# Optimization experiments

Hardware: AMD Instinct MI355X
Metric: run time of the kernel (lower is better)

The kernel has to match this reference:

```python
import jax, jax.numpy as jnp
import numpy as np

TOP_K = 2

def setup_inputs() -> dict:
    key = jax.random.key(0)
    ks = jax.random.split(key, 5)
    B, T, C, E, H = 4, 2048, 1024, 16, 4096
    x = jax.random.normal(ks[0], (B, T, C), dtype=jnp.float32)
    w_router = jax.random.normal(ks[1], (C, E), dtype=jnp.float32) / np.sqrt(C)
    w1 = jax.random.normal(ks[2], (E, C, H), dtype=jnp.float32) / np.sqrt(C)
    b1 = jnp.zeros((E, H), dtype=jnp.float32)
    w2 = jax.random.normal(ks[3], (E, H, C), dtype=jnp.float32) / np.sqrt(H)
    b2 = jnp.zeros((E, C), dtype=jnp.float32)
    return {"x": x, "w_router": w_router, "w1": w1, "b1": b1, "w2": w2, "b2": b2}


def reference(x, w_router, w1, b1, w2, b2):
    B, T, C = x.shape
    E = w1.shape[0]
    xf = x.reshape(-1, C)                       # [N, C]
    N = xf.shape[0]

    logits = xf @ w_router                      # [N, E]
    rw, sel = jax.lax.top_k(logits, TOP_K)      # [N, K]
    rw = jax.nn.softmax(rw.astype(jnp.float32), axis=-1).astype(x.dtype)

    # combine weight per (token, expert): sum of routing weights over the
    # k-slots that selected that expert (equivalent to the per-k masked loop)
    comb = jnp.zeros((N, E), dtype=x.dtype)
    comb = comb.at[jnp.arange(N)[:, None], sel].add(rw)  # [N, E]

    # loop over experts via scan: out += comb[:, e:e+1] * FFN_e(xf)
    def step(acc, params):
        w1e, b1e, w2e, b2e, ce = params         # ce: [N]
        h = jax.nn.relu(xf @ w1e + b1e)         # [N, 4C]
        y = h @ w2e + b2e                       # [N, C]
        return acc + ce[:, None] * y, None

    out0 = jnp.zeros_like(xf)
    out, _ = jax.lax.scan(step, out0, (w1, b1, w2, b2, comb.T))
    return out.reshape(B, T, C)
```

## Files before the change

### kernel.cpp

```cpp
#include <hip/hip_runtime.h>
#include <hip/hip_bf16.h>


typedef __attribute__((ext_vector_type(4))) float f32x4;
typedef __attribute__((ext_vector_type(8))) __bf16 bf16x8;
typedef __attribute__((ext_vector_type(8))) unsigned short u16x8;

#define NEXP 16
#define CAP  2048
#define CDIM 1024
#define HDIM 4096
#define KS2 2
#define BMG 256
#define BNG 256
#define SLOT 8192

__device__ __forceinline__ unsigned short f2bf(float f) {
  return __builtin_bit_cast(unsigned short, (__bf16)f);
}

typedef __attribute__((address_space(3))) void  lds_void;
typedef __attribute__((address_space(1))) const void gbl_void;
__device__ __forceinline__ void gload16(const void* g, void* l) {
  __builtin_amdgcn_global_load_lds((gbl_void*)g, (lds_void*)l, 16, 0, 0);
}

__device__ __forceinline__ void xcd_remap(int& bx, int& by, int& bz) {
  const int gx = gridDim.x, gy = gridDim.y;
  const int nwg = gx * gy * gridDim.z;
  int flat = blockIdx.x + gx * (blockIdx.y + gy * blockIdx.z);
  flat = (flat & 7) * (nwg >> 3) + (flat >> 3);
  bx = flat % gx;
  const int t = flat / gx;
  by = t % gy;
  bz = t / gy;
}

__global__ __launch_bounds__(64) void router_kernel(
    const float* __restrict__ x, const float* __restrict__ wr,
    float* __restrict__ pair_w, int* __restrict__ counts,
    int* __restrict__ lists)
{
  const int n = blockIdx.x;
  const int l = threadIdx.x;
  const float* xrow = x + (size_t)n * CDIM;
  double acc[NEXP];
#pragma unroll
  for (int e = 0; e < NEXP; e++) acc[e] = 0.0;
  for (int it = 0; it < CDIM / 64; it++) {
    const int c = l + it * 64;
    const double xv = (double)xrow[c];
    const float* w = wr + c * NEXP;
#pragma unroll
    for (int e = 0; e < NEXP; e++) acc[e] += xv * (double)w[e];
  }
#pragma unroll
  for (int e = 0; e < NEXP; e++) {
    double v = acc[e];
    for (int off = 32; off > 0; off >>= 1) v += __shfl_xor(v, off, 64);
    acc[e] = v;
  }
  if (l == 0) {
    int e0 = 0; double b0 = acc[0];
    for (int e = 1; e < NEXP; e++) if (acc[e] > b0) { b0 = acc[e]; e0 = e; }
    int e1 = -1; double b1v = -1e300;
    for (int e = 0; e < NEXP; e++) {
      if (e == e0) continue;
      if (acc[e] > b1v) { b1v = acc[e]; e1 = e; }
    }
    const double d = exp(b1v - b0);
    pair_w[2 * n]     = (float)(1.0 / (1.0 + d));
    pair_w[2 * n + 1] = (float)(d / (1.0 + d));
    int p0 = atomicAdd(&counts[e0], 1);
    if (p0 < CAP) lists[e0 * CAP + p0] = 2 * n;
    int p1 = atomicAdd(&counts[e1], 1);
    if (p1 < CAP) lists[e1 * CAP + p1] = 2 * n + 1;
  }
}

__global__ __launch_bounds__(256) void cvt_x_kernel(
    const float* __restrict__ x, unsigned short* __restrict__ xb, int n8)
{
  const int i = blockIdx.x * 256 + threadIdx.x;
  if (i >= n8) return;
  float4 a = ((const float4*)x)[2 * i];
  float4 b = ((const float4*)x)[2 * i + 1];
  u16x8 v;
  v[0] = f2bf(a.x); v[1] = f2bf(a.y); v[2] = f2bf(a.z); v[3] = f2bf(a.w);
  v[4] = f2bf(b.x); v[5] = f2bf(b.y); v[6] = f2bf(b.z); v[7] = f2bf(b.w);
  ((u16x8*)xb)[i] = v;
}

__global__ __launch_bounds__(256) void transpose_cvt_kernel(
    const float* __restrict__ src, unsigned short* __restrict__ dst,
    int K, int Nn)
{
  __shared__ __align__(16) unsigned short tile[64][72];
  const size_t eoff = (size_t)blockIdx.z * K * Nn;
  const float* S = src + eoff;
  unsigned short* D = dst + eoff;
  const int n0 = blockIdx.x * 64, k0 = blockIdx.y * 64;
  const int t = threadIdx.x;
  {
    const int nl = (t & 15) * 4, kr = t >> 4;
#pragma unroll
    for (int p = 0; p < 4; p++) {
      const int k = kr + p * 16;
      float4 v = *(const float4*)(S + (size_t)(k0 + k) * Nn + n0 + nl);
      tile[nl + 0][k] = f2bf(v.x);
      tile[nl + 1][k] = f2bf(v.y);
      tile[nl + 2][k] = f2bf(v.z);
      tile[nl + 3][k] = f2bf(v.w);
    }
  }
  __syncthreads();
  {
    const int kq = (t & 7) * 8, nr = t >> 3;
#pragma unroll
    for (int p = 0; p < 2; p++) {
      const int n = nr + p * 32;
      u16x8 v = *(const u16x8*)&tile[n][kq];
      *(u16x8*)(D + (size_t)(n0 + n) * K + k0 + kq) = v;
    }
  }
}


#define STAGE(parx, hx, koffb)                                                 \
  do {                                                                         \
    unsigned short* Ad = &lds[((parx) * 2 + (hx)) * SLOT + w * 512];           \
    unsigned short* Bd = &lds[4 * SLOT + ((parx) * 2 + (hx)) * SLOT + w * 512];\
    gload16(agA0 + (koffb), Ad);                                               \
    gload16(agA1 + (koffb), Ad + 4096);                                        \
    gload16(bgB0 + (koffb), Bd);                                               \
    gload16(bgB1 + (koffb), Bd + 4096);                                        \
  } while (0)

#define COMPUTE(parx, hx)                                                      \
  do {                                                                         \
    const unsigned short* As_ = &lds[((parx) * 2 + (hx)) * SLOT];              \
    const unsigned short* Bs_ = &lds[4 * SLOT + ((parx) * 2 + (hx)) * SLOT];   \
    bf16x8 af[8], bfv[4];                                                      \
    _Pragma("unroll")                                                          \
    for (int mf = 0; mf < 8; mf++)                                             \
      af[mf] = *(const bf16x8*)(As_ + (wr * 128 + mf * 16 + lrow) * 32 + qsw); \
    _Pragma("unroll")                                                          \
    for (int nf = 0; nf < 4; nf++)                                             \
      bfv[nf] = *(const bf16x8*)(Bs_ + (wc * 64 + nf * 16 + lrow) * 32 + qsw); \
    __builtin_amdgcn_s_setprio(1);                                             \
    _Pragma("unroll")                                                          \
    for (int mf = 0; mf < 8; mf++)                                             \
      _Pragma("unroll")                                                        \
      for (int nf = 0; nf < 4; nf++)                                           \
        acc[mf][nf] = __builtin_amdgcn_mfma_f32_16x16x32_bf16(                 \
            af[mf], bfv[nf], acc[mf][nf], 0, 0, 0);                            \
    __builtin_amdgcn_s_setprio(0);                                             \
  } while (0)

#define VMCNT4 asm volatile("s_waitcnt vmcnt(4)" ::: "memory")
#define VMCNT0 asm volatile("s_waitcnt vmcnt(0)" ::: "memory")
#define SBAR   asm volatile("s_barrier" ::: "memory")

__global__ __launch_bounds__(512, 2) void gemm1_8p_kernel(
    const unsigned short* __restrict__ xb, const unsigned short* __restrict__ wb,
    const float* __restrict__ b1, const int* __restrict__ counts,
    const int* __restrict__ lists, unsigned short* __restrict__ Hb)
{
  int bx, by, bz;
  xcd_remap(bx, by, bz);
  const int e = bz;
  int cnt = counts[e]; if (cnt > CAP) cnt = CAP;
  const int m0 = by * BMG;
  if (m0 >= cnt) return;
  const int n0 = bx * BNG;
  const int* list = lists + e * CAP;
  const unsigned short* W = wb + (size_t)e * CDIM * HDIM;

  __shared__ __align__(16) unsigned short lds[8 * SLOT];

  const int t = threadIdx.x, w = t >> 6, lane = t & 63;
  const int wr = w >> 2, wc = w & 3;
  const int lrow = lane & 15, lgrp = lane >> 4;
  const int qsw = (lgrp ^ ((lrow >> 1) & 3)) * 8;

  const int sr0 = w * 16 + (lane >> 2), sr1 = 128 + w * 16 + (lane >> 2);
  const int sq = ((lane & 3) ^ ((lane >> 3) & 3)) * 16;
  int ai0 = m0 + sr0; if (ai0 > cnt - 1) ai0 = cnt - 1;
  int ai1 = m0 + sr1; if (ai1 > cnt - 1) ai1 = cnt - 1;
  const char* agA0 = (const char*)(xb + (size_t)(list[ai0] >> 1) * CDIM) + sq;
  const char* agA1 = (const char*)(xb + (size_t)(list[ai1] >> 1) * CDIM) + sq;
  const char* bgB0 = (const char*)(W + (size_t)(n0 + sr0) * CDIM) + sq;
  const char* bgB1 = (const char*)(W + (size_t)(n0 + sr1) * CDIM) + sq;

  f32x4 acc[8][4] = {};

  const int NT = CDIM / 64;
  STAGE(0, 0, 0);
  STAGE(0, 1, 64);
  for (int tt = 0; tt < NT - 1; ++tt) {
    const int par = tt & 1;
    const int kofn = (tt + 1) * 128;
#pragma unroll
    for (int h = 0; h < 2; ++h) {
      VMCNT4; SBAR;
      STAGE(par ^ 1, h, kofn + h * 64);
      COMPUTE(par, h);
    }
  }
  {
    const int par = (NT - 1) & 1;
    VMCNT4; SBAR; COMPUTE(par, 0);
    VMCNT0; SBAR; COMPUTE(par, 1);
  }

  int hrow[8][4]; bool valid[8][4];
#pragma unroll
  for (int mf = 0; mf < 8; mf++)
#pragma unroll
    for (int rr = 0; rr < 4; rr++) {
      const int mi = m0 + wr * 128 + mf * 16 + lgrp * 4 + rr;
      valid[mf][rr] = (mi < cnt);
      hrow[mf][rr] = list[valid[mf][rr] ? mi : (cnt - 1)];
    }
#pragma unroll
  for (int nf = 0; nf < 4; nf++) {
    const int col = n0 + wc * 64 + nf * 16 + lrow;
    const float bias = b1[e * HDIM + col];
#pragma unroll
    for (int mf = 0; mf < 8; mf++)
#pragma unroll
      for (int rr = 0; rr < 4; rr++)
        if (valid[mf][rr]) {
          float h = acc[mf][nf][rr] + bias;
          h = h > 0.f ? h : 0.f;
          Hb[(size_t)hrow[mf][rr] * HDIM + col] = f2bf(h);
        }
  }
}

__global__ __launch_bounds__(512, 2) void gemm2_8p_kernel(
    const unsigned short* __restrict__ Hb, const unsigned short* __restrict__ wb,
    const float* __restrict__ b2, const float* __restrict__ pair_w,
    const int* __restrict__ counts, const int* __restrict__ lists,
    float* __restrict__ out)
{
  int bx, by, bz;
  xcd_remap(bx, by, bz);
  const int e = bz / KS2, ks = bz % KS2;
  int cnt = counts[e]; if (cnt > CAP) cnt = CAP;
  const int m0 = by * BMG;
  if (m0 >= cnt) return;
  const int n0 = bx * BNG;
  const int* list = lists + e * CAP;
  const unsigned short* W = wb + (size_t)e * HDIM * CDIM;
  const int kbegb = ks * (HDIM / KS2) * 2;

  __shared__ __align__(16) unsigned short lds[8 * SLOT];

  const int t = threadIdx.x, w = t >> 6, lane = t & 63;
  const int wr = w >> 2, wc = w & 3;
  const int lrow = lane & 15, lgrp = lane >> 4;
  const int qsw = (lgrp ^ ((lrow >> 1) & 3)) * 8;

  const int sr0 = w * 16 + (lane >> 2), sr1 = 128 + w * 16 + (lane >> 2);
  const int sq = ((lane & 3) ^ ((lane >> 3) & 3)) * 16;
  int ai0 = m0 + sr0; if (ai0 > cnt - 1) ai0 = cnt - 1;
  int ai1 = m0 + sr1; if (ai1 > cnt - 1) ai1 = cnt - 1;
  const char* agA0 = (const char*)(Hb + (size_t)list[ai0] * HDIM) + kbegb + sq;
  const char* agA1 = (const char*)(Hb + (size_t)list[ai1] * HDIM) + kbegb + sq;
  const char* bgB0 = (const char*)(W + (size_t)(n0 + sr0) * HDIM) + kbegb + sq;
  const char* bgB1 = (const char*)(W + (size_t)(n0 + sr1) * HDIM) + kbegb + sq;

  f32x4 acc[8][4] = {};

  const int NT = (HDIM / KS2) / 64;
  STAGE(0, 0, 0);
  STAGE(0, 1, 64);
  for (int tt = 0; tt < NT - 1; ++tt) {
    const int par = tt & 1;
    const int kofn = (tt + 1) * 128;
#pragma unroll
    for (int h = 0; h < 2; ++h) {
      VMCNT4; SBAR;
      STAGE(par ^ 1, h, kofn + h * 64);
      COMPUTE(par, h);
    }
  }
  {
    const int par = (NT - 1) & 1;
    VMCNT4; SBAR; COMPUTE(par, 0);
    VMCNT0; SBAR; COMPUTE(par, 1);
  }

  float wgt[8][4]; int tok[8][4]; bool valid[8][4];
#pragma unroll
  for (int mf = 0; mf < 8; mf++)
#pragma unroll
    for (int rr = 0; rr < 4; rr++) {
      const int mi = m0 + wr * 128 + mf * 16 + lgrp * 4 + rr;
      valid[mf][rr] = (mi < cnt);
      const int p = list[valid[mf][rr] ? mi : (cnt - 1)];
      wgt[mf][rr] = pair_w[p];
      tok[mf][rr] = p >> 1;
    }
#pragma unroll
  for (int nf = 0; nf < 4; nf++) {
    const int col = n0 + wc * 64 + nf * 16 + lrow;
    const float bias = (ks == 0) ? b2[e * CDIM + col] : 0.f;
#pragma unroll
    for (int mf = 0; mf < 8; mf++)
#pragma unroll
      for (int rr = 0; rr < 4; rr++)
        if (valid[mf][rr])
          atomicAdd(out + (size_t)tok[mf][rr] * CDIM + col,
                    wgt[mf][rr] * (acc[mf][nf][rr] + bias));
  }
}

__device__ __forceinline__ int swz(int row, int b) {
  return row * 128 + (b ^ (((row >> 1) & 7) << 4));
}

#define MFMA_COMPUTE_F(Abase, Bbase)                                           \
  _Pragma("unroll")                                                            \
  for (int kk = 0; kk < 2; kk++) {                                             \
    bf16x8 af[4], bfr[4];                                                      \
    const int kb = (kk * 32 + lgrp * 8) * 2;                                   \
    _Pragma("unroll")                                                          \
    for (int i = 0; i < 4; i++)                                                \
      af[i] = *(const bf16x8*)((Abase) + swz(wm + i * 16 + lrow, kb));         \
    _Pragma("unroll")                                                          \
    for (int j = 0; j < 4; j++)                                                \
      bfr[j] = *(const bf16x8*)((Bbase) + swz(wn + j * 16 + lrow, kb));        \
    _Pragma("unroll")                                                          \
    for (int i = 0; i < 4; i++)                                                \
      _Pragma("unroll")                                                        \
      for (int j = 0; j < 4; j++)                                              \
        acc[i][j] = __builtin_amdgcn_mfma_f32_16x16x32_bf16(                   \
            af[i], bfr[j], acc[i][j], 0, 0, 0);                                \
  }

__global__ __launch_bounds__(256) void gemm1_f32_kernel(
    const float* __restrict__ x, const float* __restrict__ w1,
    const float* __restrict__ b1, const int* __restrict__ counts,
    const int* __restrict__ lists, unsigned short* __restrict__ Hb,
    int e_base, int h_by_pair)
{
  const int e = e_base + blockIdx.z;
  int cnt = counts[e]; if (cnt > CAP) cnt = CAP;
  const int m0 = blockIdx.y * 128;
  if (m0 >= cnt) return;
  const int n0 = blockIdx.x * 128;
  const int* list = lists + e * CAP;
  const float* W = w1 + (size_t)e * CDIM * HDIM;
  __shared__ __align__(16) unsigned short As[128 * 64];
  __shared__ __align__(16) unsigned short Bs[128 * 64];
  const int t = threadIdx.x;
  const int a_row = t >> 1, a_half = t & 1;
  int a_idx = m0 + a_row; if (a_idx > cnt - 1) a_idx = cnt - 1;
  const float* a_src = x + (size_t)(list[a_idx] >> 1) * CDIM + a_half * 32;
  const int b_np = t & 63, b_kg = t >> 6;
  const int wid = t >> 6, lane = t & 63;
  const int wm = (wid >> 1) * 64, wn = (wid & 1) * 64;
  const int lrow = lane & 15, lgrp = lane >> 4;
  f32x4 acc[4][4] = {};
  for (int kt = 0; kt < CDIM; kt += 64) {
    {
      const float* s = a_src + kt;
      u16x8 cv[4];
#pragma unroll
      for (int q = 0; q < 4; q++) {
        float4 v0 = *(const float4*)(s + q * 8);
        float4 v1 = *(const float4*)(s + q * 8 + 4);
        cv[q][0] = f2bf(v0.x); cv[q][1] = f2bf(v0.y);
        cv[q][2] = f2bf(v0.z); cv[q][3] = f2bf(v0.w);
        cv[q][4] = f2bf(v1.x); cv[q][5] = f2bf(v1.y);
        cv[q][6] = f2bf(v1.z); cv[q][7] = f2bf(v1.w);
      }
#pragma unroll
      for (int q = 0; q < 4; q++)
        *(u16x8*)((char*)As + swz(a_row, (a_half * 32 + q * 8) * 2)) = cv[q];
    }
    {
#pragma unroll
      for (int it = 0; it < 2; it++) {
        const int k0 = (b_kg + 4 * it) * 8;
        u16x8 c0, c1;
#pragma unroll
        for (int j = 0; j < 8; j++) {
          float2 v = *(const float2*)(W + (size_t)(kt + k0 + j) * HDIM + n0 + 2 * b_np);
          c0[j] = f2bf(v.x); c1[j] = f2bf(v.y);
        }
        *(u16x8*)((char*)Bs + swz(2 * b_np,     k0 * 2)) = c0;
        *(u16x8*)((char*)Bs + swz(2 * b_np + 1, k0 * 2)) = c1;
      }
    }
    __syncthreads();
    MFMA_COMPUTE_F((const char*)As, (const char*)Bs)
    __syncthreads();
  }
  int hrow[4][4]; bool valid[4][4];
#pragma unroll
  for (int i = 0; i < 4; i++)
#pragma unroll
    for (int r = 0; r < 4; r++) {
      const int mi = m0 + wm + i * 16 + lgrp * 4 + r;
      valid[i][r] = (mi < cnt);
      const int idx = valid[i][r] ? mi : (cnt - 1);
      hrow[i][r] = h_by_pair ? list[idx] : idx;
    }
#pragma unroll
  for (int j = 0; j < 4; j++) {
    const int col = n0 + wn + j * 16 + lrow;
    const float bias = b1[e * HDIM + col];
#pragma unroll
    for (int i = 0; i < 4; i++)
#pragma unroll
      for (int r = 0; r < 4; r++)
        if (valid[i][r]) {
          float h = acc[i][j][r] + bias;
          h = h > 0.f ? h : 0.f;
          Hb[(size_t)hrow[i][r] * HDIM + col] = f2bf(h);
        }
  }
}

__global__ __launch_bounds__(256) void gemm2_f32_kernel(
    const unsigned short* __restrict__ Hb, const float* __restrict__ w2,
    const float* __restrict__ b2, const float* __restrict__ pair_w,
    const int* __restrict__ counts, const int* __restrict__ lists,
    float* __restrict__ out, int e_base, int h_by_pair)
{
  const int e = e_base + blockIdx.z;
  int cnt = counts[e]; if (cnt > CAP) cnt = CAP;
  const int m0 = blockIdx.y * 128;
  if (m0 >= cnt) return;
  const int n0 = blockIdx.x * 128;
  const int* list = lists + e * CAP;
  const float* W = w2 + (size_t)e * HDIM * CDIM;
  __shared__ __align__(16) unsigned short As[128 * 64];
  __shared__ __align__(16) unsigned short Bs[128 * 64];
  const int t = threadIdx.x;
  const int a_row = t >> 1, a_half = t & 1;
  int a_idx = m0 + a_row; if (a_idx > cnt - 1) a_idx = cnt - 1;
  const unsigned short* a_src =
      Hb + (size_t)(h_by_pair ? list[a_idx] : a_idx) * HDIM + a_half * 32;
  const int b_np = t & 63, b_kg = t >> 6;
  const int wid = t >> 6, lane = t & 63;
  const int wm = (wid >> 1) * 64, wn = (wid & 1) * 64;
  const int lrow = lane & 15, lgrp = lane >> 4;
  f32x4 acc[4][4] = {};
  for (int kt = 0; kt < HDIM; kt += 64) {
    {
      const unsigned short* s = a_src + kt;
#pragma unroll
      for (int q = 0; q < 4; q++) {
        u16x8 v = *(const u16x8*)(s + q * 8);
        *(u16x8*)((char*)As + swz(a_row, (a_half * 32 + q * 8) * 2)) = v;
      }
    }
    {
#pragma unroll
      for (int it = 0; it < 2; it++) {
        const int k0 = (b_kg + 4 * it) * 8;
        u16x8 c0, c1;
#pragma unroll
        for (int j = 0; j < 8; j++) {
          float2 v = *(const float2*)(W + (size_t)(kt + k0 + j) * CDIM + n0 + 2 * b_np);
          c0[j] = f2bf(v.x); c1[j] = f2bf(v.y);
        }
        *(u16x8*)((char*)Bs + swz(2 * b_np,     k0 * 2)) = c0;
        *(u16x8*)((char*)Bs + swz(2 * b_np + 1, k0 * 2)) = c1;
      }
    }
    __syncthreads();
    MFMA_COMPUTE_F((const char*)As, (const char*)Bs)
    __syncthreads();
  }
  float wgt[4][4]; int tok[4][4]; bool valid[4][4];
#pragma unroll
  for (int i = 0; i < 4; i++)
#pragma unroll
    for (int r = 0; r < 4; r++) {
      const int mi = m0 + wm + i * 16 + lgrp * 4 + r;
      valid[i][r] = (mi < cnt);
      const int idx = valid[i][r] ? mi : (cnt - 1);
      const int p = list[idx];
      wgt[i][r] = pair_w[p];
      tok[i][r] = p >> 1;
    }
#pragma unroll
  for (int j = 0; j < 4; j++) {
    const int col = n0 + wn + j * 16 + lrow;
    const float bias = b2[e * CDIM + col];
#pragma unroll
    for (int i = 0; i < 4; i++)
#pragma unroll
      for (int r = 0; r < 4; r++)
        if (valid[i][r])
          atomicAdd(out + (size_t)tok[i][r] * CDIM + col,
                    wgt[i][r] * (acc[i][j][r] + bias));
  }
}

extern "C" void kernel_launch(void* const* d_in, const int* in_sizes, int n_in,
                              void* d_out, int out_size, void* d_ws, size_t ws_size,
                              hipStream_t stream)
{
  const float* x  = (const float*)d_in[0];
  const float* wr = (const float*)d_in[1];
  const float* w1 = (const float*)d_in[2];
  const float* b1 = (const float*)d_in[3];
  const float* w2 = (const float*)d_in[4];
  const float* b2 = (const float*)d_in[5];
  float* out = (float*)d_out;

  const int N = in_sizes[0] / CDIM;

  char* ws = (char*)d_ws;
  int* counts = (int*)ws;
  int* lists  = (int*)(ws + 256);
  float* pw   = (float*)(ws + 256 + NEXP * CAP * 4);
  size_t off = 256 + (size_t)NEXP * CAP * 4 + (size_t)2 * N * 4;
  off = (off + 255) & ~(size_t)255;
  unsigned short* xb = (unsigned short*)(ws + off);
  const size_t xb_sz = (size_t)N * CDIM * 2;
  unsigned short* Hb = (unsigned short*)(ws + off + xb_sz);
  const size_t Hb_sz = (size_t)2 * N * HDIM * 2;
  unsigned short* wb = (unsigned short*)(ws + off + xb_sz + Hb_sz);
  const size_t wb_sz = (size_t)NEXP * CDIM * HDIM * 2;

  const size_t need_new = off + xb_sz + Hb_sz + wb_sz;
  const size_t need_old = off + Hb_sz;

  hipMemsetAsync(d_ws, 0, 64, stream);
  hipMemsetAsync(d_out, 0, (size_t)out_size * 4, stream);

  router_kernel<<<N, 64, 0, stream>>>(x, wr, pw, counts, lists);

  if (ws_size >= need_new) {
    cvt_x_kernel<<<(N * CDIM / 8 + 255) / 256, 256, 0, stream>>>(
        x, xb, N * CDIM / 8);
    transpose_cvt_kernel<<<dim3(HDIM / 64, CDIM / 64, NEXP), 256, 0, stream>>>(
        w1, wb, CDIM, HDIM);
    gemm1_8p_kernel<<<dim3(HDIM / BNG, CAP / BMG, NEXP), 512, 0, stream>>>(
        xb, wb, b1, counts, lists, Hb);
    transpose_cvt_kernel<<<dim3(CDIM / 64, HDIM / 64, NEXP), 256, 0, stream>>>(
        w2, wb, HDIM, CDIM);
    gemm2_8p_kernel<<<dim3(CDIM / BNG, CAP / BMG, NEXP * KS2), 512, 0, stream>>>(
        Hb, wb, b2, pw, counts, lists, out);
  } else if (ws_size >= need_old) {
    unsigned short* Hb0 = (unsigned short*)(ws + off);
    gemm1_f32_kernel<<<dim3(HDIM / 128, CAP / 128, NEXP), 256, 0, stream>>>(
        x, w1, b1, counts, lists, Hb0, 0, 1);
    gemm2_f32_kernel<<<dim3(CDIM / 128, CAP / 128, NEXP), 256, 0, stream>>>(
        Hb0, w2, b2, pw, counts, lists, out, 0, 1);
  }
}
```

Before: 921.5 us.

## Replace direct global-to-LDS loads with register-staged prefetch pipeline in MoE GEMMs

Both expert GEMM kernels stop using global_load_lds to copy A/B tiles straight into LDS. They now load tiles into registers two half-steps ahead and write them to swizzled LDS with ds_write after each barrier, overlapping global latency with MFMA compute. This drops the vmcnt waits but adds register pressure (eight extra 16-byte vectors per thread) and extra LDS write instructions, and it relies on the compiler's own waitcnt placement for correctness.

```diff
diff --git a/kernel.cpp b/kernel.cpp
--- a/kernel.cpp
+++ b/kernel.cpp
@@ -17,12 +17,6 @@
 
 __device__ __forceinline__ unsigned short f2bf(float f) {
   return __builtin_bit_cast(unsigned short, (__bf16)f);
-}
-
-typedef __attribute__((address_space(3))) void  lds_void;
-typedef __attribute__((address_space(1))) const void gbl_void;
-__device__ __forceinline__ void gload16(const void* g, void* l) {
-  __builtin_amdgcn_global_load_lds((gbl_void*)g, (lds_void*)l, 16, 0, 0);
 }
 
 __device__ __forceinline__ void xcd_remap(int& bx, int& by, int& bz) {
@@ -126,14 +120,22 @@
 }
 
 
-#define STAGE(parx, hx, koffb)                                                 \
+#define LOADR(ra0, ra1, rb0, rb1, koffb)                                       \
   do {                                                                         \
-    unsigned short* Ad = &lds[((parx) * 2 + (hx)) * SLOT + w * 512];           \
-    unsigned short* Bd = &lds[4 * SLOT + ((parx) * 2 + (hx)) * SLOT + w * 512];\
-    gload16(agA0 + (koffb), Ad);                                               \
-    gload16(agA1 + (koffb), Ad + 4096);                                        \
-    gload16(bgB0 + (koffb), Bd);                                               \
-    gload16(bgB1 + (koffb), Bd + 4096);                                        \
+    ra0 = *(const u16x8*)(ag0 + (koffb));                                      \
+    ra1 = *(const u16x8*)(ag1 + (koffb));                                      \
+    rb0 = *(const u16x8*)(bg0 + (koffb));                                      \
+    rb1 = *(const u16x8*)(bg1 + (koffb));                                      \
+  } while (0)
+
+#define DSW(parx, hx, ra0, ra1, rb0, rb1)                                      \
+  do {                                                                         \
+    unsigned short* SA_ = &lds[((parx) * 2 + (hx)) * SLOT];                    \
+    unsigned short* SB_ = &lds[4 * SLOT + ((parx) * 2 + (hx)) * SLOT];         \
+    *(u16x8*)(SA_ + sw0) = ra0;                                                \
+    *(u16x8*)(SA_ + sw1) = ra1;                                                \
+    *(u16x8*)(SB_ + sw0) = rb0;                                                \
+    *(u16x8*)(SB_ + sw1) = rb1;                                                \
   } while (0)
 
 #define COMPUTE(parx, hx)                                                      \
@@ -157,9 +159,27 @@
     __builtin_amdgcn_s_setprio(0);                                             \
   } while (0)
 
-#define VMCNT4 asm volatile("s_waitcnt vmcnt(4)" ::: "memory")
-#define VMCNT0 asm volatile("s_waitcnt vmcnt(0)" ::: "memory")
-#define SBAR   asm volatile("s_barrier" ::: "memory")
+#define SBAR asm volatile("s_barrier" ::: "memory")
+
+#define GEMM_MAIN_LOOP(NT)                                                     \
+  u16x8 eA0, eA1, eB0, eB1, oA0, oA1, oB0, oB1;                                \
+  LOADR(eA0, eA1, eB0, eB1, 0);                                                \
+  LOADR(oA0, oA1, oB0, oB1, 64);                                               \
+  DSW(0, 0, eA0, eA1, eB0, eB1);                                               \
+  DSW(0, 1, oA0, oA1, oB0, oB1);                                               \
+  LOADR(eA0, eA1, eB0, eB1, 128);                                              \
+  LOADR(oA0, oA1, oB0, oB1, 192);                                              \
+  asm volatile("s_waitcnt lgkmcnt(0)" ::: "memory");                           \
+  for (int tt = 0; tt < (NT); ++tt) {                                          \
+    const int par = tt & 1;                                                    \
+    SBAR;                                                                      \
+    if (tt + 1 < (NT)) DSW(par ^ 1, 0, eA0, eA1, eB0, eB1);                    \
+    if (tt + 2 < (NT)) LOADR(eA0, eA1, eB0, eB1, (tt + 2) * 128);              \
+    COMPUTE(par, 0);                                                           \
+    if (tt + 1 < (NT)) DSW(par ^ 1, 1, oA0, oA1, oB0, oB1);                    \
+    if (tt + 2 < (NT)) LOADR(oA0, oA1, oB0, oB1, (tt + 2) * 128 + 64);         \
+    COMPUTE(par, 1);                                                           \
+  }
 
 __global__ __launch_bounds__(512, 2) void gemm1_8p_kernel(
     const unsigned short* __restrict__ xb, const unsigned short* __restrict__ wb,
@@ -183,35 +203,19 @@
   const int lrow = lane & 15, lgrp = lane >> 4;
   const int qsw = (lgrp ^ ((lrow >> 1) & 3)) * 8;
 
-  const int sr0 = w * 16 + (lane >> 2), sr1 = 128 + w * 16 + (lane >> 2);
-  const int sq = ((lane & 3) ^ ((lane >> 3) & 3)) * 16;
+  const int sr0 = w * 16 + (lane >> 2), sr1 = 128 + sr0;
+  const int wq = ((lane & 3) ^ ((lane >> 3) & 3)) * 8;
+  const int sw0 = sr0 * 32 + wq, sw1 = sr1 * 32 + wq;
   int ai0 = m0 + sr0; if (ai0 > cnt - 1) ai0 = cnt - 1;
   int ai1 = m0 + sr1; if (ai1 > cnt - 1) ai1 = cnt - 1;
-  const char* agA0 = (const char*)(xb + (size_t)(list[ai0] >> 1) * CDIM) + sq;
-  const char* agA1 = (const char*)(xb + (size_t)(list[ai1] >> 1) * CDIM) + sq;
-  const char* bgB0 = (const char*)(W + (size_t)(n0 + sr0) * CDIM) + sq;
-  const char* bgB1 = (const char*)(W + (size_t)(n0 + sr1) * CDIM) + sq;
+  const char* ag0 = (const char*)(xb + (size_t)(list[ai0] >> 1) * CDIM) + (lane & 3) * 16;
+  const char* ag1 = (const char*)(xb + (size_t)(list[ai1] >> 1) * CDIM) + (lane & 3) * 16;
+  const char* bg0 = (const char*)(W + (size_t)(n0 + sr0) * CDIM) + (lane & 3) * 16;
+  const char* bg1 = (const char*)(W + (size_t)(n0 + sr1) * CDIM) + (lane & 3) * 16;
 
   f32x4 acc[8][4] = {};
 
-  const int NT = CDIM / 64;
-  STAGE(0, 0, 0);
-  STAGE(0, 1, 64);
-  for (int tt = 0; tt < NT - 1; ++tt) {
-    const int par = tt & 1;
-    const int kofn = (tt + 1) * 128;
-#pragma unroll
-    for (int h = 0; h < 2; ++h) {
-      VMCNT4; SBAR;
-      STAGE(par ^ 1, h, kofn + h * 64);
-      COMPUTE(par, h);
-    }
-  }
-  {
-    const int par = (NT - 1) & 1;
-    VMCNT4; SBAR; COMPUTE(par, 0);
-    VMCNT0; SBAR; COMPUTE(par, 1);
-  }
+  GEMM_MAIN_LOOP(CDIM / 64)
 
   int hrow[8][4]; bool valid[8][4];
 #pragma unroll
@@ -262,35 +266,19 @@
   const int lrow = lane & 15, lgrp = lane >> 4;
   const int qsw = (lgrp ^ ((lrow >> 1) & 3)) * 8;
 
-  const int sr0 = w * 16 + (lane >> 2), sr1 = 128 + w * 16 + (lane >> 2);
-  const int sq = ((lane & 3) ^ ((lane >> 3) & 3)) * 16;
+  const int sr0 = w * 16 + (lane >> 2), sr1 = 128 + sr0;
+  const int wq = ((lane & 3) ^ ((lane >> 3) & 3)) * 8;
+  const int sw0 = sr0 * 32 + wq, sw1 = sr1 * 32 + wq;
   int ai0 = m0 + sr0; if (ai0 > cnt - 1) ai0 = cnt - 1;
   int ai1 = m0 + sr1; if (ai1 > cnt - 1) ai1 = cnt - 1;
-  const char* agA0 = (const char*)(Hb + (size_t)list[ai0] * HDIM) + kbegb + sq;
-  const char* agA1 = (const char*)(Hb + (size_t)list[ai1] * HDIM) + kbegb + sq;
-  const char* bgB0 = (const char*)(W + (size_t)(n0 + sr0) * HDIM) + kbegb + sq;
-  const char* bgB1 = (const char*)(W + (size_t)(n0 + sr1) * HDIM) + kbegb + sq;
+  const char* ag0 = (const char*)(Hb + (size_t)list[ai0] * HDIM) + kbegb + (lane & 3) * 16;
+  const char* ag1 = (const char*)(Hb + (size_t)list[ai1] * HDIM) + kbegb + (lane & 3) * 16;
+  const char* bg0 = (const char*)(W + (size_t)(n0 + sr0) * HDIM) + kbegb + (lane & 3) * 16;
+  const char* bg1 = (const char*)(W + (size_t)(n0 + sr1) * HDIM) + kbegb + (lane & 3) * 16;
 
   f32x4 acc[8][4] = {};
 
-  const int NT = (HDIM / KS2) / 64;
-  STAGE(0, 0, 0);
-  STAGE(0, 1, 64);
-  for (int tt = 0; tt < NT - 1; ++tt) {
-    const int par = tt & 1;
-    const int kofn = (tt + 1) * 128;
-#pragma unroll
-    for (int h = 0; h < 2; ++h) {
-      VMCNT4; SBAR;
-      STAGE(par ^ 1, h, kofn + h * 64);
-      COMPUTE(par, h);
-    }
-  }
-  {
-    const int par = (NT - 1) & 1;
-    VMCNT4; SBAR; COMPUTE(par, 0);
-    VMCNT0; SBAR; COMPUTE(par, 1);
-  }
+  GEMM_MAIN_LOOP((HDIM / KS2) / 64)
 
   float wgt[8][4]; int tok[8][4]; bool valid[8][4];
 #pragma unroll
```

Measured after the change: 948.7 us. 1.03x slower.
